# Kernel tuning notes

Measured on AMD Instinct MI355X. Metric: run time of the kernel, lower is better.

The kernel has to match this reference:

```python
import jax, jax.numpy as jnp
import numpy as np
from jax import lax

T, IN, H, OUT = 4096, 32, 512, 32


def _lstm_layer(x_seq, W_ih, W_hh, b_ih, b_hh):
    # x_seq: [T, D_in]; PyTorch gate order: i, f, g, o
    Hd = W_hh.shape[1]
    b = b_ih + b_hh

    def step(carry, x):
        h, c = carry
        gates = x @ W_ih.T + h @ W_hh.T + b  # [4H]
        i, f, g, o = jnp.split(gates, 4)
        i = jax.nn.sigmoid(i)
        f = jax.nn.sigmoid(f)
        g = jnp.tanh(g)
        o = jax.nn.sigmoid(o)
        c2 = f * c + i * g
        h2 = o * jnp.tanh(c2)
        return (h2, c2), h2

    init = (jnp.zeros((Hd,), x_seq.dtype), jnp.zeros((Hd,), x_seq.dtype))
    _, hs = lax.scan(step, init, x_seq)
    return hs  # [T, Hd]


def setup_inputs() -> dict:
    key = jax.random.key(0)
    ks = jax.random.split(key, 16)
    s = 0.05
    return {
        "seq": jax.random.normal(ks[0], (T, IN), jnp.float32),
        "W_ih1": jax.random.normal(ks[1], (4 * H, IN), jnp.float32) * s,
        "W_hh1": jax.random.normal(ks[2], (4 * H, H), jnp.float32) * s,
        "b_ih1": jax.random.normal(ks[3], (4 * H,), jnp.float32) * s,
        "b_hh1": jax.random.normal(ks[4], (4 * H,), jnp.float32) * s,
        "W_ih2": jax.random.normal(ks[5], (4 * H, H), jnp.float32) * s,
        "W_hh2": jax.random.normal(ks[6], (4 * H, H), jnp.float32) * s,
        "b_ih2": jax.random.normal(ks[7], (4 * H,), jnp.float32) * s,
        "b_hh2": jax.random.normal(ks[8], (4 * H,), jnp.float32) * s,
        "W_ih3": jax.random.normal(ks[9], (4 * H, H), jnp.float32) * s,
        "W_hh3": jax.random.normal(ks[10], (4 * H, H), jnp.float32) * s,
        "b_ih3": jax.random.normal(ks[11], (4 * H,), jnp.float32) * s,
        "b_hh3": jax.random.normal(ks[12], (4 * H,), jnp.float32) * s,
        "W_out": jax.random.normal(ks[13], (OUT, H), jnp.float32) * s,
        "b_out": jax.random.normal(ks[14], (OUT,), jnp.float32) * s,
    }


def reference(seq, W_ih1, W_hh1, b_ih1, b_hh1, W_ih2, W_hh2, b_ih2, b_hh2,
              W_ih3, W_hh3, b_ih3, b_hh3, W_out, b_out):
    h1 = _lstm_layer(seq, W_ih1, W_hh1, b_ih1, b_hh1)  # [T, H]
    h2 = _lstm_layer(h1, W_ih2, W_hh2, b_ih2, b_hh2)   # [T, H]
    h3 = _lstm_layer(h2, W_ih3, W_hh3, b_ih3, b_hh3)   # [T, H]
    return h3 @ W_out.T + b_out  # [T, OUT]
```

## Files before the change

### kernel.cpp

```cpp
#include <hip/hip_runtime.h>


#define T_SEQ 4096
#define HDIM  512
#define NWG_L 32
#define NTH   1024

typedef unsigned long long u64;

__device__ __forceinline__ u64 cohLoad(const u64* p) {
    return __hip_atomic_load(p, __ATOMIC_RELAXED, __HIP_MEMORY_SCOPE_AGENT);
}
__device__ __forceinline__ void cohStore(u64* p, u64 v) {
    __hip_atomic_store(p, v, __ATOMIC_RELAXED, __HIP_MEMORY_SCOPE_AGENT);
}
__device__ __forceinline__ float fsigmoid(float x) {
    return __builtin_amdgcn_rcpf(1.f + __expf(-x));
}
__device__ __forceinline__ float ftanh(float x) {
    float e = __expf(2.f * fabsf(x));
    float t = 1.f - 2.f * __builtin_amdgcn_rcpf(e + 1.f);
    return copysignf(t, x);
}
__device__ __forceinline__ float bcast(float v, int k) {
    return __uint_as_float(__builtin_amdgcn_readlane(__float_as_uint(v), k));
}

template <int BM, int BN, int BK>
__global__ __launch_bounds__(256)
void gemm_abt(const float* __restrict__ A, const float* __restrict__ B,
              const float* __restrict__ bias1,
              float* __restrict__ C, int M, int N, int K) {
    constexpr int NTX = BN / 4;
    constexpr int NTY = 256 / NTX;
    constexpr int TM  = BM / NTY;
    __shared__ float As[BM][BK + 1];
    __shared__ float Bs[BN][BK + 1];

    const int tid = threadIdx.x;
    const int tx = tid % NTX;
    const int ty = tid / NTX;
    const int m0 = blockIdx.y * BM;
    const int n0 = blockIdx.x * BN;

    float acc[TM][4];
    #pragma unroll
    for (int i = 0; i < TM; ++i)
        #pragma unroll
        for (int j = 0; j < 4; ++j) acc[i][j] = 0.f;

    for (int k0 = 0; k0 < K; k0 += BK) {
        constexpr int AV = BM * BK / 4;
        #pragma unroll
        for (int i = tid; i < AV; i += 256) {
            int r = i / (BK / 4), c4 = i % (BK / 4);
            float4 v = *(const float4*)(A + (size_t)(m0 + r) * K + k0 + c4 * 4);
            As[r][c4 * 4 + 0] = v.x; As[r][c4 * 4 + 1] = v.y;
            As[r][c4 * 4 + 2] = v.z; As[r][c4 * 4 + 3] = v.w;
        }
        constexpr int BV = BN * BK / 4;
        #pragma unroll
        for (int i = tid; i < BV; i += 256) {
            int r = i / (BK / 4), c4 = i % (BK / 4);
            float4 v = *(const float4*)(B + (size_t)(n0 + r) * K + k0 + c4 * 4);
            Bs[r][c4 * 4 + 0] = v.x; Bs[r][c4 * 4 + 1] = v.y;
            Bs[r][c4 * 4 + 2] = v.z; Bs[r][c4 * 4 + 3] = v.w;
        }
        __syncthreads();
        #pragma unroll
        for (int kk = 0; kk < BK; ++kk) {
            float a[TM], b[4];
            #pragma unroll
            for (int i = 0; i < TM; ++i) a[i] = As[ty * TM + i][kk];
            #pragma unroll
            for (int j = 0; j < 4; ++j) b[j] = Bs[tx * 4 + j][kk];
            #pragma unroll
            for (int i = 0; i < TM; ++i)
                #pragma unroll
                for (int j = 0; j < 4; ++j) acc[i][j] += a[i] * b[j];
        }
        __syncthreads();
    }

    #pragma unroll
    for (int j = 0; j < 4; ++j) {
        float bv = bias1 ? bias1[n0 + tx * 4 + j] : 0.f;
        #pragma unroll
        for (int i = 0; i < TM; ++i) acc[i][j] += bv;
    }
    #pragma unroll
    for (int i = 0; i < TM; ++i) {
        int m = m0 + ty * TM + i;
        float4 v = make_float4(acc[i][0], acc[i][1], acc[i][2], acc[i][3]);
        *(float4*)(C + (size_t)m * N + n0 + tx * 4) = v;
    }
}

__global__ void unpack_h(const u64* __restrict__ hp, float* __restrict__ out,
                         int n) {
    int i = blockIdx.x * blockDim.x + threadIdx.x;
    if (i < n) out[i] = __uint_as_float((unsigned)hp[i]);
}

__global__ __launch_bounds__(NTH, 4)
void lstm_fused(const float* __restrict__ seq,
                const float* __restrict__ Wih1, const float* __restrict__ Whh1,
                const float* __restrict__ bih1, const float* __restrict__ bhh1,
                const float* __restrict__ Wih2, const float* __restrict__ Whh2,
                const float* __restrict__ bih2, const float* __restrict__ bhh2,
                const float* __restrict__ Wih3, const float* __restrict__ Whh3,
                const float* __restrict__ bih3, const float* __restrict__ bhh3,
                u64* __restrict__ hp) {
    __shared__ float part[2][NTH];

    const int blk   = blockIdx.x;
    const int layer = blk >> 5;
    const int g     = blk & 31;
    const int tid   = threadIdx.x;
    const int wv    = tid >> 6;
    const int lane  = tid & 63;
    const int grow  = (lane >> 4) * HDIM + g * 16 + (lane & 15);

    const float* Wih = layer == 0 ? Wih1 : (layer == 1 ? Wih2 : Wih3);
    const float* Whh = layer == 0 ? Whh1 : (layer == 1 ? Whh2 : Whh3);
    const float* bih = layer == 0 ? bih1 : (layer == 1 ? bih2 : bih3);
    const float* bhh = layer == 0 ? bhh1 : (layer == 1 ? bhh2 : bhh3);

    float w[64];
    #pragma unroll
    for (int m = 0; m < 64; ++m) w[m] = 0.f;
    if (layer == 0) {
        const float* wp = Whh + (size_t)grow * HDIM + wv * 32;
        #pragma unroll
        for (int i = 0; i < 8; ++i) {
            float4 v = ((const float4*)wp)[i];
            w[4*i+0]=v.x; w[4*i+1]=v.y; w[4*i+2]=v.z; w[4*i+3]=v.w;
        }
        w[32] = Wih[(size_t)grow * 32 + 2 * wv + 0];
        w[33] = Wih[(size_t)grow * 32 + 2 * wv + 1];
    } else {
        const float* wp = (wv < 8)
            ? Wih + (size_t)grow * HDIM + wv * 64
            : Whh + (size_t)grow * HDIM + (wv - 8) * 64;
        #pragma unroll
        for (int i = 0; i < 16; ++i) {
            float4 v = ((const float4*)wp)[i];
            w[4*i+0]=v.x; w[4*i+1]=v.y; w[4*i+2]=v.z; w[4*i+3]=v.w;
        }
    }
    #pragma unroll
    for (int m = 0; m < 64; ++m) asm volatile("" : "+v"(w[m]));

    const float brow = bih[grow] + bhh[grow];

    u64*       hpOwn   = hp + (size_t)layer * T_SEQ * HDIM;
    u64*       hpX     = hp + (size_t)3 * T_SEQ * HDIM;
    u64*       hpXOwn  = hpX + (size_t)layer * T_SEQ * HDIM;
    const u64* hpPrevX = hpX + (size_t)(layer > 0 ? layer - 1 : 0) * T_SEQ * HDIM;

    float c = 0.f;

    for (unsigned t = 0; t < T_SEQ; ++t) {
        const int pb = t & 1;

        float hval = 0.f;
        float xval = 0.f;
        if (layer == 0) {
            if (lane < 32 && t > 0) {
                const u64* ph = hpOwn + (size_t)(t - 1) * HDIM + wv * 32 + lane;
                u64 v;
                do { v = cohLoad(ph); } while ((unsigned)(v >> 32) != t);
                hval = __uint_as_float((unsigned)v);
            }
            if (lane >= 32 && lane < 34)
                xval = seq[(size_t)t * 32 + 2 * wv + (lane - 32)];
        } else {
            if (wv < 8) {
                const u64* px = hpPrevX + (size_t)t * HDIM + wv * 64 + lane;
                u64 v;
                do { v = cohLoad(px); } while ((unsigned)(v >> 32) != t + 1u);
                hval = __uint_as_float((unsigned)v);
            } else if (t > 0) {
                const u64* ph = hpOwn + (size_t)(t - 1) * HDIM
                              + (wv - 8) * 64 + lane;
                u64 v;
                do { v = cohLoad(ph); } while ((unsigned)(v >> 32) != t);
                hval = __uint_as_float((unsigned)v);
            }
        }

        float pe = 0.f, po = 0.f;
        if (layer == 0) {
            #pragma unroll
            for (int k = 0; k < 32; k += 2) {
                pe = fmaf(bcast(hval, k),     w[k],     pe);
                po = fmaf(bcast(hval, k + 1), w[k + 1], po);
            }
            pe = fmaf(bcast(xval, 32), w[32], pe);
            po = fmaf(bcast(xval, 33), w[33], po);
        } else {
            #pragma unroll
            for (int k = 0; k < 64; k += 2) {
                pe = fmaf(bcast(hval, k),     w[k],     pe);
                po = fmaf(bcast(hval, k + 1), w[k + 1], po);
            }
        }
        part[pb][wv * 64 + lane] = pe + po;
        __syncthreads();

        if (wv == 0) {
            float tot = brow;
            #pragma unroll
            for (int wvv = 0; wvv < 16; ++wvv) tot += part[pb][wvv * 64 + lane];
            const int c16 = lane & 15;
            float ai = __shfl(tot, c16 +  0, 64);
            float af = __shfl(tot, c16 + 16, 64);
            float ag = __shfl(tot, c16 + 32, 64);
            float ao = __shfl(tot, c16 + 48, 64);
            if (lane < 32) {
                float iv = fsigmoid(ai);
                float fv = fsigmoid(af);
                float gv = ftanh(ag);
                float ov = fsigmoid(ao);
                c = fv * c + iv * gv;
                float h = ov * ftanh(c);
                u64 pkt = (u64)__float_as_uint(h) | ((u64)(t + 1u) << 32);
                if (lane < 16)
                    cohStore(hpOwn + (size_t)t * HDIM + g * 16 + lane, pkt);
                else if (layer < 2)
                    cohStore(hpXOwn + (size_t)t * HDIM + g * 16 + (lane - 16),
                             pkt);
            }
        }
    }
}

extern "C" void kernel_launch(void* const* d_in, const int* in_sizes, int n_in,
                              void* d_out, int out_size, void* d_ws, size_t ws_size,
                              hipStream_t stream) {
    const float* seq   = (const float*)d_in[0];
    const float* W_ih1 = (const float*)d_in[1];
    const float* W_hh1 = (const float*)d_in[2];
    const float* b_ih1 = (const float*)d_in[3];
    const float* b_hh1 = (const float*)d_in[4];
    const float* W_ih2 = (const float*)d_in[5];
    const float* W_hh2 = (const float*)d_in[6];
    const float* b_ih2 = (const float*)d_in[7];
    const float* b_hh2 = (const float*)d_in[8];
    const float* W_ih3 = (const float*)d_in[9];
    const float* W_hh3 = (const float*)d_in[10];
    const float* b_ih3 = (const float*)d_in[11];
    const float* b_hh3 = (const float*)d_in[12];
    const float* W_out = (const float*)d_in[13];
    const float* b_out = (const float*)d_in[14];
    float* out = (float*)d_out;

    u64*   hp   = (u64*)d_ws;
    float* hs2f = (float*)d_ws;
    const u64* hp2 = hp + (size_t)2 * T_SEQ * HDIM;

    hipMemsetAsync(hp, 0, (size_t)5 * T_SEQ * HDIM * sizeof(u64), stream);

    lstm_fused<<<3 * NWG_L, NTH, 0, stream>>>(
        seq, W_ih1, W_hh1, b_ih1, b_hh1, W_ih2, W_hh2, b_ih2, b_hh2,
        W_ih3, W_hh3, b_ih3, b_hh3, hp);

    const int n = T_SEQ * HDIM;
    unpack_h<<<(n + 255) / 256, 256, 0, stream>>>(hp2, hs2f, n);

    gemm_abt<64, 32, 32><<<dim3(1, T_SEQ / 64), 256, 0, stream>>>(
        hs2f, W_out, b_out, out, T_SEQ, 32, HDIM);
}
```

Measured before the change: 6.167 ms.

## Fuse output projection into persistent LSTM kernel and add double-buffered h mailbox

Adds 32 extra workgroups to the persistent LSTM kernel. Each one waits on the tagged layer-3 hidden states for a 128-row chunk and computes the output projection while the recurrence is still running. This removes the separate unpack and GEMM launches from the tail of the run. Half of each layer's workgroups also read the previous h from a small double-buffered mailbox instead of the full history array, which is meant to spread polling traffic. The risks are that the spinning GEMM blocks compete for memory bandwidth with the latency-critical recurrence, and that correctness depends on all workgroups being co-resident.

```diff
diff --git a/kernel.cpp b/kernel.cpp
--- a/kernel.cpp
+++ b/kernel.cpp
@@ -5,6 +5,7 @@
 #define HDIM  512
 #define NWG_L 32
 #define NTH   1024
+#define NWG_G 32
 
 typedef unsigned long long u64;
 
@@ -24,82 +25,6 @@
 }
 __device__ __forceinline__ float bcast(float v, int k) {
     return __uint_as_float(__builtin_amdgcn_readlane(__float_as_uint(v), k));
-}
-
-template <int BM, int BN, int BK>
-__global__ __launch_bounds__(256)
-void gemm_abt(const float* __restrict__ A, const float* __restrict__ B,
-              const float* __restrict__ bias1,
-              float* __restrict__ C, int M, int N, int K) {
-    constexpr int NTX = BN / 4;
-    constexpr int NTY = 256 / NTX;
-    constexpr int TM  = BM / NTY;
-    __shared__ float As[BM][BK + 1];
-    __shared__ float Bs[BN][BK + 1];
-
-    const int tid = threadIdx.x;
-    const int tx = tid % NTX;
-    const int ty = tid / NTX;
-    const int m0 = blockIdx.y * BM;
-    const int n0 = blockIdx.x * BN;
-
-    float acc[TM][4];
-    #pragma unroll
-    for (int i = 0; i < TM; ++i)
-        #pragma unroll
-        for (int j = 0; j < 4; ++j) acc[i][j] = 0.f;
-
-    for (int k0 = 0; k0 < K; k0 += BK) {
-        constexpr int AV = BM * BK / 4;
-        #pragma unroll
-        for (int i = tid; i < AV; i += 256) {
-            int r = i / (BK / 4), c4 = i % (BK / 4);
-            float4 v = *(const float4*)(A + (size_t)(m0 + r) * K + k0 + c4 * 4);
-            As[r][c4 * 4 + 0] = v.x; As[r][c4 * 4 + 1] = v.y;
-            As[r][c4 * 4 + 2] = v.z; As[r][c4 * 4 + 3] = v.w;
-        }
-        constexpr int BV = BN * BK / 4;
-        #pragma unroll
-        for (int i = tid; i < BV; i += 256) {
-            int r = i / (BK / 4), c4 = i % (BK / 4);
-            float4 v = *(const float4*)(B + (size_t)(n0 + r) * K + k0 + c4 * 4);
-            Bs[r][c4 * 4 + 0] = v.x; Bs[r][c4 * 4 + 1] = v.y;
-            Bs[r][c4 * 4 + 2] = v.z; Bs[r][c4 * 4 + 3] = v.w;
-        }
-        __syncthreads();
-        #pragma unroll
-        for (int kk = 0; kk < BK; ++kk) {
-            float a[TM], b[4];
-            #pragma unroll
-            for (int i = 0; i < TM; ++i) a[i] = As[ty * TM + i][kk];
-            #pragma unroll
-            for (int j = 0; j < 4; ++j) b[j] = Bs[tx * 4 + j][kk];
-            #pragma unroll
-            for (int i = 0; i < TM; ++i)
-                #pragma unroll
-                for (int j = 0; j < 4; ++j) acc[i][j] += a[i] * b[j];
-        }
-        __syncthreads();
-    }
-
-    #pragma unroll
-    for (int j = 0; j < 4; ++j) {
-        float bv = bias1 ? bias1[n0 + tx * 4 + j] : 0.f;
-        #pragma unroll
-        for (int i = 0; i < TM; ++i) acc[i][j] += bv;
-    }
-    #pragma unroll
-    for (int i = 0; i < TM; ++i) {
-        int m = m0 + ty * TM + i;
-        float4 v = make_float4(acc[i][0], acc[i][1], acc[i][2], acc[i][3]);
-        *(float4*)(C + (size_t)m * N + n0 + tx * 4) = v;
-    }
-}
-
-__global__ void unpack_h(const u64* __restrict__ hp, float* __restrict__ out,
-                         int n) {
-    int i = blockIdx.x * blockDim.x + threadIdx.x;
-    if (i < n) out[i] = __uint_as_float((unsigned)hp[i]);
 }
 
 __global__ __launch_bounds__(NTH, 4)
@@ -110,13 +35,72 @@
                 const float* __restrict__ bih2, const float* __restrict__ bhh2,
                 const float* __restrict__ Wih3, const float* __restrict__ Whh3,
                 const float* __restrict__ bih3, const float* __restrict__ bhh3,
+                const float* __restrict__ Wout, const float* __restrict__ bout,
+                float* __restrict__ out,
                 u64* __restrict__ hp) {
     __shared__ float part[2][NTH];
-
-    const int blk   = blockIdx.x;
+    __shared__ float As[128][33];
+    __shared__ float Bs[32][33];
+
+    const int blk = blockIdx.x;
+    const int tid = threadIdx.x;
+
+    u64* const mbB = hp + (size_t)5 * T_SEQ * HDIM;
+
+    if (blk >= 3 * NWG_L) {
+        const u64* __restrict__ hp2 = hp + (size_t)2 * T_SEQ * HDIM;
+        const int m0 = (blk - 3 * NWG_L) * 128;
+        const int tx = tid & 7;
+        const int ty = tid >> 3;
+
+        {
+            const u64* gp = hp2 + (size_t)(m0 + 127) * HDIM + (tid & 511);
+            const unsigned want = (unsigned)(m0 + 128);
+            while ((unsigned)(cohLoad(gp) >> 32) != want)
+                __builtin_amdgcn_s_sleep(127);
+        }
+        __syncthreads();
+
+        float a0 = 0.f, a1 = 0.f, a2 = 0.f, a3 = 0.f;
+        for (int k0 = 0; k0 < HDIM; k0 += 32) {
+            #pragma unroll
+            for (int i = tid; i < 2048; i += NTH) {
+                const int r = i >> 4, c2 = i & 15;
+                const u64* ap = hp2 + (size_t)(m0 + r) * HDIM + k0 + c2 * 2;
+                const unsigned want = (unsigned)(m0 + r + 1);
+                u64 v0 = cohLoad(ap), v1 = cohLoad(ap + 1);
+                while ((unsigned)(v0 >> 32) != want ||
+                       (unsigned)(v1 >> 32) != want) {
+                    v0 = cohLoad(ap); v1 = cohLoad(ap + 1);
+                }
+                As[r][c2 * 2 + 0] = __uint_as_float((unsigned)v0);
+                As[r][c2 * 2 + 1] = __uint_as_float((unsigned)v1);
+            }
+            if (tid < 256) {
+                const int r = tid >> 3, c4 = tid & 7;
+                float4 v = *(const float4*)(Wout + (size_t)r * HDIM + k0 + c4 * 4);
+                Bs[r][c4 * 4 + 0] = v.x; Bs[r][c4 * 4 + 1] = v.y;
+                Bs[r][c4 * 4 + 2] = v.z; Bs[r][c4 * 4 + 3] = v.w;
+            }
+            __syncthreads();
+            #pragma unroll
+            for (int kk = 0; kk < 32; ++kk) {
+                const float a = As[ty][kk];
+                a0 = fmaf(a, Bs[tx * 4 + 0][kk], a0);
+                a1 = fmaf(a, Bs[tx * 4 + 1][kk], a1);
+                a2 = fmaf(a, Bs[tx * 4 + 2][kk], a2);
+                a3 = fmaf(a, Bs[tx * 4 + 3][kk], a3);
+            }
+            __syncthreads();
+        }
+        float4 v = make_float4(a0 + bout[tx * 4 + 0], a1 + bout[tx * 4 + 1],
+                               a2 + bout[tx * 4 + 2], a3 + bout[tx * 4 + 3]);
+        *(float4*)(out + (size_t)(m0 + ty) * 32 + tx * 4) = v;
+        return;
+    }
+
     const int layer = blk >> 5;
     const int g     = blk & 31;
-    const int tid   = threadIdx.x;
     const int wv    = tid >> 6;
     const int lane  = tid & 63;
     const int grow  = (lane >> 4) * HDIM + g * 16 + (lane & 15);
@@ -157,6 +141,9 @@
     u64*       hpX     = hp + (size_t)3 * T_SEQ * HDIM;
     u64*       hpXOwn  = hpX + (size_t)layer * T_SEQ * HDIM;
     const u64* hpPrevX = hpX + (size_t)(layer > 0 ? layer - 1 : 0) * T_SEQ * HDIM;
+    u64*       mbOwn   = mbB + (size_t)layer * 2 * HDIM;
+
+    const bool useB = (g >= 16);
 
     float c = 0.f;
 
@@ -167,7 +154,9 @@
         float xval = 0.f;
         if (layer == 0) {
             if (lane < 32 && t > 0) {
-                const u64* ph = hpOwn + (size_t)(t - 1) * HDIM + wv * 32 + lane;
+                const u64* ph = useB
+                    ? mbOwn + (size_t)((t - 1) & 1) * HDIM + wv * 32 + lane
+                    : hpOwn + (size_t)(t - 1) * HDIM + wv * 32 + lane;
                 u64 v;
                 do { v = cohLoad(ph); } while ((unsigned)(v >> 32) != t);
                 hval = __uint_as_float((unsigned)v);
@@ -181,8 +170,9 @@
                 do { v = cohLoad(px); } while ((unsigned)(v >> 32) != t + 1u);
                 hval = __uint_as_float((unsigned)v);
             } else if (t > 0) {
-                const u64* ph = hpOwn + (size_t)(t - 1) * HDIM
-                              + (wv - 8) * 64 + lane;
+                const u64* ph = useB
+                    ? mbOwn + (size_t)((t - 1) & 1) * HDIM + (wv - 8) * 64 + lane
+                    : hpOwn + (size_t)(t - 1) * HDIM + (wv - 8) * 64 + lane;
                 u64 v;
                 do { v = cohLoad(ph); } while ((unsigned)(v >> 32) != t);
                 hval = __uint_as_float((unsigned)v);
@@ -217,20 +207,21 @@
             float af = __shfl(tot, c16 + 16, 64);
             float ag = __shfl(tot, c16 + 32, 64);
             float ao = __shfl(tot, c16 + 48, 64);
-            if (lane < 32) {
-                float iv = fsigmoid(ai);
-                float fv = fsigmoid(af);
-                float gv = ftanh(ag);
-                float ov = fsigmoid(ao);
-                c = fv * c + iv * gv;
-                float h = ov * ftanh(c);
-                u64 pkt = (u64)__float_as_uint(h) | ((u64)(t + 1u) << 32);
-                if (lane < 16)
-                    cohStore(hpOwn + (size_t)t * HDIM + g * 16 + lane, pkt);
-                else if (layer < 2)
-                    cohStore(hpXOwn + (size_t)t * HDIM + g * 16 + (lane - 16),
-                             pkt);
-            }
+            float iv = fsigmoid(ai);
+            float fv = fsigmoid(af);
+            float gv = ftanh(ag);
+            float ov = fsigmoid(ao);
+            c = fv * c + iv * gv;
+            float h = ov * ftanh(c);
+            u64 pkt = (u64)__float_as_uint(h) | ((u64)(t + 1u) << 32);
+            if (lane < 16)
+                cohStore(hpOwn + (size_t)t * HDIM + g * 16 + lane, pkt);
+            else if (lane < 32)
+                cohStore(mbOwn + (size_t)(t & 1) * HDIM + g * 16 + (lane - 16),
+                         pkt);
+            else if (lane < 48 && layer < 2)
+                cohStore(hpXOwn + (size_t)t * HDIM + g * 16 + (lane - 32),
+                         pkt);
         }
     }
 }
@@ -255,19 +246,11 @@
     const float* b_out = (const float*)d_in[14];
     float* out = (float*)d_out;
 
-    u64*   hp   = (u64*)d_ws;
-    float* hs2f = (float*)d_ws;
-    const u64* hp2 = hp + (size_t)2 * T_SEQ * HDIM;
-
-    hipMemsetAsync(hp, 0, (size_t)5 * T_SEQ * HDIM * sizeof(u64), stream);
-
-    lstm_fused<<<3 * NWG_L, NTH, 0, stream>>>(
+    u64* hp = (u64*)d_ws;
+    const size_t WS_U64 = (size_t)5 * T_SEQ * HDIM + (size_t)3 * 2 * HDIM;
+    hipMemsetAsync(hp, 0, WS_U64 * sizeof(u64), stream);
+
+    lstm_fused<<<3 * NWG_L + NWG_G, NTH, 0, stream>>>(
         seq, W_ih1, W_hh1, b_ih1, b_hh1, W_ih2, W_hh2, b_ih2, b_hh2,
-        W_ih3, W_hh3, b_ih3, b_hh3, hp);
-
-    const int n = T_SEQ * HDIM;
-    unpack_h<<<(n + 255) / 256, 256, 0, stream>>>(hp2, hs2f, n);
-
-    gemm_abt<64, 32, 32><<<dim3(1, T_SEQ / 64), 256, 0, stream>>>(
-        hs2f, W_out, b_out, out, T_SEQ, 32, HDIM);
-}
+        W_ih3, W_hh3, b_ih3, b_hh3, W_out, b_out, out, hp);
+}
```

Result: slower. 6.472 ms (+4.9%).
